# Optimization experiments

Measured on AMD Instinct MI355X. Metric: run time of the kernel, lower is better.

The kernel has to match this reference:

```python
import jax, jax.numpy as jnp
import numpy as np

B, N, C, H, S = 8, 1024, 768, 8, 16  # C = 3 * S * S, head_dim = C // H
NCH = 3
D = C // H
SCALE = D ** -0.5
REATTEN_SCALE = 1.0  # transform_scale=False
EPS = 1e-5  # BatchNorm2d eps


def conv3x3(x, w, b):
    # x: (B*N, 3, S, S); w: (O=3, I=3, 3, 3) OIHW; 'same' padding
    y = jax.lax.conv_general_dilated(x, w, (1, 1), 'SAME',
                                     dimension_numbers=('NCHW', 'OIHW', 'NCHW'))
    return y + b[None, :, None, None]


def setup_inputs() -> dict:
    key = jax.random.key(0)
    ks = jax.random.split(key, 8)
    return {
        'x': jax.random.normal(ks[0], (B, N, C), jnp.float32),
        'qw': jax.random.normal(ks[1], (NCH, NCH, 3, 3), jnp.float32) * 0.1,
        'qb': jnp.zeros((NCH,), jnp.float32),
        'kw': jax.random.normal(ks[2], (NCH, NCH, 3, 3), jnp.float32) * 0.1,
        'kb': jnp.zeros((NCH,), jnp.float32),
        'vw': jax.random.normal(ks[3], (NCH, NCH, 3, 3), jnp.float32) * 0.1,
        'vb': jnp.zeros((NCH,), jnp.float32),
        'rw': jax.random.normal(ks[4], (H, H), jnp.float32) * 0.2,  # 1x1 conv over heads
        'rb': jnp.zeros((H,), jnp.float32),
        'bn_g': jnp.ones((H,), jnp.float32),
        'bn_b': jnp.zeros((H,), jnp.float32),
        'bn_m': jnp.zeros((H,), jnp.float32),   # running mean
        'bn_v': jnp.ones((H,), jnp.float32),    # running var
        'pw': jax.random.normal(ks[5], (C, C), jnp.float32) * 0.02,
        'pb': jnp.zeros((C,), jnp.float32),
    }


def reference(x, qw, qb, kw, kb, vw, vb, rw, rb, bn_g, bn_b, bn_m, bn_v, pw, pb):
    Bx, Nx, Cx = x.shape
    xs = x.reshape(Bx * Nx, NCH, S, S)  # unflatten; all (b, n) convs batched at once

    def heads(y):  # (B*N, 3, S, S) -> (B, H, N, D)
        return y.reshape(Bx, Nx, H, D).transpose(0, 2, 1, 3)

    q = heads(conv3x3(xs, qw, qb))
    k = heads(conv3x3(xs, kw, kb))
    v = heads(conv3x3(xs, vw, vb))

    attn = jnp.einsum('bhnd,bhmd->bhnm', q, k) * SCALE  # (B, H, N, N)
    attn = jax.nn.softmax(attn, axis=-1)
    # re-attention: 1x1 conv across heads, then BatchNorm2d (eval, running stats)
    attn = jnp.einsum('oh,bhnm->bonm', rw, attn) + rb[None, :, None, None]
    inv = (bn_g / jnp.sqrt(bn_v + EPS))[None, :, None, None]
    attn = (attn - bn_m[None, :, None, None]) * inv + bn_b[None, :, None, None]
    attn = attn * REATTEN_SCALE

    out = jnp.einsum('bhnm,bhmd->bhnd', attn, v)  # (B, H, N, D)
    out = out.transpose(0, 2, 1, 3).reshape(Bx, Nx, Cx)
    out = out @ pw.T + pb
    return (out, attn)
```

## Files before the change

### kernel.cpp

```cpp
#include <hip/hip_runtime.h>
#include <math.h>

#define B_ 8
#define N_ 1024
#define C_ 768
#define H_ 8
#define D_ 96
#define SCALE_F 0.1020620726159657f

typedef unsigned short u16;
typedef __bf16 bf16x8 __attribute__((ext_vector_type(8)));
typedef float f32x4 __attribute__((ext_vector_type(4)));
typedef u16 u16x8 __attribute__((ext_vector_type(8)));

#define MFMA(a, b, c) __builtin_amdgcn_mfma_f32_16x16x32_bf16(a, b, c, 0, 0, 0)

__device__ inline void split1(float x, u16& h, u16& l) {
    __bf16 hb = (__bf16)x;
    float hf = (float)hb;
    __bf16 lb = (__bf16)(x - hf);
    h = __builtin_bit_cast(u16, hb);
    l = __builtin_bit_cast(u16, lb);
}

__device__ inline void split4(float4 x, ushort4& h, ushort4& l) {
    split1(x.x, h.x, l.x);
    split1(x.y, h.y, l.y);
    split1(x.z, h.z, l.z);
    split1(x.w, h.w, l.w);
}

__device__ inline void bar_lds() {
    asm volatile("s_waitcnt lgkmcnt(0)" ::: "memory");
    __builtin_amdgcn_s_barrier();
}

__device__ inline float bf16_to_f32(u16 u) {
    return __builtin_bit_cast(float, (unsigned)u << 16);
}

__global__ __launch_bounds__(256) void conv_qkv(
    const float* __restrict__ x,
    const float* __restrict__ qw, const float* __restrict__ qb,
    const float* __restrict__ kw, const float* __restrict__ kb,
    const float* __restrict__ vw, const float* __restrict__ vb,
    u16* __restrict__ qh, u16* __restrict__ ql,
    u16* __restrict__ kh, u16* __restrict__ kl,
    float* __restrict__ v)
{
    __shared__ float simg[768];
    __shared__ float sw[243];
    __shared__ float sb[9];
    const int img = blockIdx.x;
    const int b = img >> 10;
    const int tid = threadIdx.x;

    for (int i = tid; i < 768; i += 256) simg[i] = x[(size_t)img * 768 + i];
    if (tid < 243) {
        int g = tid / 81, i = tid % 81;
        const float* w = (g == 0) ? qw : (g == 1) ? kw : vw;
        sw[tid] = w[i];
    }
    if (tid < 9) {
        int g = tid / 3, i = tid % 3;
        const float* bb = (g == 0) ? qb : (g == 1) ? kb : vb;
        sb[tid] = bb[i];
    }
    __syncthreads();

    const int n = img & 1023;
    for (int e = tid; e < 2304; e += 256) {
        int g = e / 768, c = e % 768;
        int oc = c >> 8, rem = c & 255, y = rem >> 4, xx = rem & 15;
        float acc = sb[g * 3 + oc];
        const float* wg = &sw[g * 81 + oc * 27];
        #pragma unroll
        for (int ic = 0; ic < 3; ++ic)
            #pragma unroll
            for (int ky = 0; ky < 3; ++ky) {
                int yy = y + ky - 1;
                if (yy < 0 || yy > 15) continue;
                #pragma unroll
                for (int kx = 0; kx < 3; ++kx) {
                    int xp = xx + kx - 1;
                    if (xp < 0 || xp > 15) continue;
                    acc += wg[ic * 9 + ky * 3 + kx] * simg[ic * 256 + yy * 16 + xp];
                }
            }
        int hh = c / 96, d = c % 96;
        size_t o = ((size_t)(b * 8 + hh) * 1024 + n) * 96 + d;
        if (g == 2) {
            v[o] = acc;
        } else {
            u16 hi, lo;
            split1(acc, hi, lo);
            if (g == 0) { qh[o] = hi; ql[o] = lo; }
            else        { kh[o] = hi; kl[o] = lo; }
        }
    }
}

__global__ __launch_bounds__(256) void vt_split(
    const float* __restrict__ v, u16* __restrict__ vt_h)
{
    __shared__ float t32[32][36];
    const int bh = blockIdx.z, n0 = blockIdx.x * 32, d0 = blockIdx.y * 32;
    const int tid = threadIdx.x;
    {
        int nn = tid >> 3, c4 = (tid & 7) * 4;
        float4 x = *(const float4*)&v[((size_t)bh * 1024 + n0 + nn) * 96 + d0 + c4];
        t32[nn][c4] = x.x; t32[nn][c4 + 1] = x.y;
        t32[nn][c4 + 2] = x.z; t32[nn][c4 + 3] = x.w;
    }
    __syncthreads();
    {
        int d = tid >> 3, n4 = (tid & 7) * 4;
        ushort4 h;
        h.x = __builtin_bit_cast(u16, (__bf16)t32[n4][d]);
        h.y = __builtin_bit_cast(u16, (__bf16)t32[n4 + 1][d]);
        h.z = __builtin_bit_cast(u16, (__bf16)t32[n4 + 2][d]);
        h.w = __builtin_bit_cast(u16, (__bf16)t32[n4 + 3][d]);
        size_t o = ((size_t)bh * 96 + d0 + d) * 1024 + n0 + n4;
        *(ushort4*)&vt_h[o] = h;
    }
}

__global__ __launch_bounds__(256) void pw_split(
    const float* __restrict__ pw, u16* __restrict__ pwh, u16* __restrict__ pwl)
{
    int i = blockIdx.x * 256 + threadIdx.x;
    float4 x = *(const float4*)&pw[(size_t)i * 4];
    ushort4 h, l;
    split4(x, h, l);
    *(ushort4*)&pwh[(size_t)i * 4] = h;
    *(ushort4*)&pwl[(size_t)i * 4] = l;
}

__global__ __launch_bounds__(512) void fused_attn(
    const u16* __restrict__ qh, const u16* __restrict__ ql,
    const u16* __restrict__ kh, const u16* __restrict__ kl,
    const u16* __restrict__ vth,
    const float* __restrict__ rw, const float* __restrict__ rb,
    const float* __restrict__ bn_g, const float* __restrict__ bn_b,
    const float* __restrict__ bn_m, const float* __restrict__ bn_v,
    float* __restrict__ attn, u16* __restrict__ o1h, u16* __restrict__ o1l)
{
    __shared__ u16 p_lds[2][32][33][8];
    __shared__ u16 m_lds[2][8][32][40];
    __shared__ float s_w2[8][8];
    __shared__ float s_b2[8];

    const int bid = blockIdx.x;
    const int b = bid & 7;
    const int n0 = (bid >> 3) * 32;
    const int tid = threadIdx.x, wid = tid >> 6, lane = tid & 63;
    const int l16 = lane & 15, kg = lane >> 4;
    const int h = wid;
    const size_t bh = (size_t)(b * 8 + h);

    if (tid < 64) {
        int o = tid >> 3, hh = tid & 7;
        float inv = bn_g[o] * rsqrtf(bn_v[o] + 1e-5f);
        s_w2[o][hh] = rw[o * 8 + hh] * inv;
        if (hh == 0) s_b2[o] = (rb[o] - bn_m[o]) * inv + bn_b[o];
    }

    bf16x8 qhf[2][3], qlf[2][3];
    #pragma unroll
    for (int nf = 0; nf < 2; ++nf)
        #pragma unroll
        for (int ks = 0; ks < 3; ++ks) {
            size_t off = (bh * 1024 + n0 + nf * 16 + l16) * 96 + ks * 32 + kg * 8;
            qhf[nf][ks] = *(const bf16x8*)&qh[off];
            qlf[nf][ks] = *(const bf16x8*)&ql[off];
        }

    float ls[2][4];
    #pragma unroll
    for (int nf = 0; nf < 2; ++nf)
        #pragma unroll
        for (int r = 0; r < 4; ++r) ls[nf][r] = 0.f;

    #pragma unroll 1
    for (int mt = 0; mt < 16; ++mt) {
        const int m0 = mt * 64;
        f32x4 sacc[2][4];
        #pragma unroll
        for (int nf = 0; nf < 2; ++nf)
            #pragma unroll
            for (int mf = 0; mf < 4; ++mf) sacc[nf][mf] = (f32x4){0.f, 0.f, 0.f, 0.f};

        __builtin_amdgcn_s_setprio(1);
        #pragma unroll
        for (int ks = 0; ks < 3; ++ks) {
            bf16x8 kbh[4];
            #pragma unroll
            for (int mf = 0; mf < 4; ++mf) {
                size_t off = (bh * 1024 + m0 + mf * 16 + l16) * 96 + ks * 32 + kg * 8;
                kbh[mf] = *(const bf16x8*)&kh[off];
            }
            #pragma unroll
            for (int nf = 0; nf < 2; ++nf)
                #pragma unroll
                for (int mf = 0; mf < 4; ++mf)
                    sacc[nf][mf] = MFMA(qhf[nf][ks], kbh[mf], sacc[nf][mf]);
        }
        __builtin_amdgcn_s_setprio(0);

        #pragma unroll
        for (int nf = 0; nf < 2; ++nf)
            #pragma unroll
            for (int mf = 0; mf < 4; ++mf)
                #pragma unroll
                for (int r = 0; r < 4; ++r)
                    ls[nf][r] += __expf(sacc[nf][mf][r] * SCALE_F);
    }

    float rv[2][4];
    #pragma unroll
    for (int nf = 0; nf < 2; ++nf)
        #pragma unroll
        for (int r = 0; r < 4; ++r) {
            float s = ls[nf][r];
            #pragma unroll
            for (int off = 1; off < 16; off <<= 1) s += __shfl_xor(s, off);
            rv[nf][r] = 1.0f / s;
        }

    __syncthreads();

    float w2all[8][8], b2r[8];
    #pragma unroll
    for (int o = 0; o < 8; ++o) {
        b2r[o] = s_b2[o];
        #pragma unroll
        for (int hh = 0; hh < 8; ++hh) w2all[o][hh] = s_w2[o][hh];
    }

    f32x4 pvacc[2][6];
    #pragma unroll
    for (int nf = 0; nf < 2; ++nf)
        #pragma unroll
        for (int df = 0; df < 6; ++df) pvacc[nf][df] = (f32x4){0.f, 0.f, 0.f, 0.f};

    const int mm = lane & 31, halfq = lane >> 5;
    const int nlA = wid * 4 + halfq;
    const int nlB = wid * 4 + 2 + halfq;

#define QKEXP(MT, BUF)                                                          \
    {                                                                           \
        const int m0_ = (MT) * 32;                                              \
        f32x4 sacc_[2][2];                                                      \
        _Pragma("unroll")                                                       \
        for (int nf_ = 0; nf_ < 2; ++nf_)                                       \
            _Pragma("unroll")                                                   \
            for (int mf_ = 0; mf_ < 2; ++mf_)                                   \
                sacc_[nf_][mf_] = (f32x4){0.f, 0.f, 0.f, 0.f};                  \
        __builtin_amdgcn_s_setprio(1);                                          \
        _Pragma("unroll")                                                       \
        for (int ks_ = 0; ks_ < 3; ++ks_) {                                     \
            bf16x8 kbh_[2], kbl_[2];                                            \
            _Pragma("unroll")                                                   \
            for (int mf_ = 0; mf_ < 2; ++mf_) {                                 \
                size_t off_ = (bh * 1024 + m0_ + mf_ * 16 + l16) * 96 + ks_ * 32 + kg * 8; \
                kbh_[mf_] = *(const bf16x8*)&kh[off_];                          \
                kbl_[mf_] = *(const bf16x8*)&kl[off_];                          \
            }                                                                   \
            _Pragma("unroll")                                                   \
            for (int nf_ = 0; nf_ < 2; ++nf_)                                   \
                _Pragma("unroll")                                               \
                for (int mf_ = 0; mf_ < 2; ++mf_) {                             \
                    sacc_[nf_][mf_] = MFMA(qhf[nf_][ks_], kbh_[mf_], sacc_[nf_][mf_]); \
                    sacc_[nf_][mf_] = MFMA(qhf[nf_][ks_], kbl_[mf_], sacc_[nf_][mf_]); \
                    sacc_[nf_][mf_] = MFMA(qlf[nf_][ks_], kbh_[mf_], sacc_[nf_][mf_]); \
                }                                                               \
        }                                                                       \
        __builtin_amdgcn_s_setprio(0);                                          \
        _Pragma("unroll")                                                       \
        for (int nf_ = 0; nf_ < 2; ++nf_)                                       \
            _Pragma("unroll")                                                   \
            for (int mf_ = 0; mf_ < 2; ++mf_)                                   \
                _Pragma("unroll")                                               \
                for (int r_ = 0; r_ < 4; ++r_) {                                \
                    float pp_ = __expf(sacc_[nf_][mf_][r_] * SCALE_F) * rv[nf_][r_]; \
                    p_lds[BUF][nf_ * 16 + kg * 4 + r_][mf_ * 16 + l16][h] =     \
                        __builtin_bit_cast(u16, (__bf16)pp_);                   \
                }                                                               \
    }

    QKEXP(0, 0)
    bar_lds();

    #pragma unroll 1
    for (int mt = 0; mt < 32; ++mt) {
        const int m0 = mt * 32;
        const int buf = mt & 1;

        bf16x8 vbh[6];
        #pragma unroll
        for (int df = 0; df < 6; ++df) {
            size_t off = (bh * 96 + df * 16 + l16) * 1024 + m0 + kg * 8;
            vbh[df] = *(const bf16x8*)&vth[off];
        }

        if (mt < 31) QKEXP(mt + 1, buf ^ 1)

        {
            u16x8 pa = *(const u16x8*)&p_lds[buf][nlA][mm][0];
            u16x8 pb = *(const u16x8*)&p_lds[buf][nlB][mm][0];
            float macc[2][8];
            #pragma unroll
            for (int o = 0; o < 8; ++o) { macc[0][o] = b2r[o]; macc[1][o] = b2r[o]; }
            #pragma unroll
            for (int hh = 0; hh < 8; ++hh) {
                float pA = bf16_to_f32(pa[hh]);
                float pB = bf16_to_f32(pb[hh]);
                #pragma unroll
                for (int o = 0; o < 8; ++o) {
                    macc[0][o] += w2all[o][hh] * pA;
                    macc[1][o] += w2all[o][hh] * pB;
                }
            }
            #pragma unroll
            for (int o = 0; o < 8; ++o) {
                size_t basео = ((size_t)(b * 8 + o) * 1024 + n0);
                __builtin_nontemporal_store(macc[0][o],
                    &attn[(basео + nlA) * 1024 + m0 + mm]);
                __builtin_nontemporal_store(macc[1][o],
                    &attn[(basео + nlB) * 1024 + m0 + mm]);
                m_lds[buf][o][nlA][mm] = __builtin_bit_cast(u16, (__bf16)macc[0][o]);
                m_lds[buf][o][nlB][mm] = __builtin_bit_cast(u16, (__bf16)macc[1][o]);
            }
        }

        bar_lds();

        bf16x8 mah[2];
        #pragma unroll
        for (int nf = 0; nf < 2; ++nf)
            mah[nf] = __builtin_bit_cast(bf16x8,
                *(const u16x8*)&m_lds[buf][wid][nf * 16 + l16][kg * 8]);
        __builtin_amdgcn_s_setprio(1);
        #pragma unroll
        for (int df = 0; df < 6; ++df)
            #pragma unroll
            for (int nf = 0; nf < 2; ++nf)
                pvacc[nf][df] = MFMA(mah[nf], vbh[df], pvacc[nf][df]);
        __builtin_amdgcn_s_setprio(0);
    }
#undef QKEXP

    #pragma unroll
    for (int nf = 0; nf < 2; ++nf)
        #pragma unroll
        for (int df = 0; df < 6; ++df)
            #pragma unroll
            for (int r = 0; r < 4; ++r) {
                int row = n0 + nf * 16 + kg * 4 + r;
                int col = h * 96 + df * 16 + l16;
                u16 hh2, ll2;
                split1(pvacc[nf][df][r], hh2, ll2);
                size_t o = ((size_t)b * 1024 + row) * 768 + col;
                o1h[o] = hh2;
                o1l[o] = ll2;
            }
}

__global__ __launch_bounds__(256) void proj_mfma(
    const u16* __restrict__ o1h, const u16* __restrict__ o1l,
    const u16* __restrict__ pwh, const u16* __restrict__ pwl,
    const float* __restrict__ pb, float* __restrict__ out)
{
    __shared__ __align__(16) u16 Ahs[5120], Als[5120];
    __shared__ __align__(16) u16 Bhs[2560], Bls[2560];
    const int t0 = blockIdx.y * 128, o0 = blockIdx.x * 64;
    const int tid = threadIdx.x;
    const int wid = tid >> 6, lane = tid & 63;
    const int l16 = lane & 15, kg = lane >> 4;
    const int wr = wid >> 1, wc = wid & 1;

    f32x4 acc[4][2];
    #pragma unroll
    for (int i = 0; i < 4; ++i)
        #pragma unroll
        for (int j = 0; j < 2; ++j) acc[i][j] = (f32x4){0.f, 0.f, 0.f, 0.f};

    for (int s = 0; s < 24; ++s) {
        const int kc = s * 32;
        if (s) __syncthreads();
        #pragma unroll
        for (int i = 0; i < 4; ++i) {
            int idx = tid + i * 256;
            int r = idx >> 3, c4 = idx & 7;
            *(ushort4*)&Ahs[r * 40 + c4 * 4] = *(const ushort4*)&o1h[(size_t)(t0 + r) * 768 + kc + c4 * 4];
            *(ushort4*)&Als[r * 40 + c4 * 4] = *(const ushort4*)&o1l[(size_t)(t0 + r) * 768 + kc + c4 * 4];
        }
        #pragma unroll
        for (int i = 0; i < 2; ++i) {
            int idx = tid + i * 256;
            int r = idx >> 3, c4 = idx & 7;
            *(ushort4*)&Bhs[r * 40 + c4 * 4] = *(const ushort4*)&pwh[(size_t)(o0 + r) * 768 + kc + c4 * 4];
            *(ushort4*)&Bls[r * 40 + c4 * 4] = *(const ushort4*)&pwl[(size_t)(o0 + r) * 768 + kc + c4 * 4];
        }
        __syncthreads();

        bf16x8 ah[4], al[4], bh8[2], bl8[2];
        #pragma unroll
        for (int f = 0; f < 4; ++f) {
            int ra = (wr * 64 + f * 16 + l16) * 40 + kg * 8;
            ah[f] = *(const bf16x8*)&Ahs[ra];
            al[f] = *(const bf16x8*)&Als[ra];
        }
        #pragma unroll
        for (int j = 0; j < 2; ++j) {
            int rb = (wc * 32 + j * 16 + l16) * 40 + kg * 8;
            bh8[j] = *(const bf16x8*)&Bhs[rb];
            bl8[j] = *(const bf16x8*)&Bls[rb];
        }
        #pragma unroll
        for (int i = 0; i < 4; ++i)
            #pragma unroll
            for (int j = 0; j < 2; ++j) {
                acc[i][j] = MFMA(ah[i], bh8[j], acc[i][j]);
                acc[i][j] = MFMA(ah[i], bl8[j], acc[i][j]);
                acc[i][j] = MFMA(al[i], bh8[j], acc[i][j]);
            }
    }

    #pragma unroll
    for (int i = 0; i < 4; ++i) {
        int rr = t0 + wr * 64 + i * 16 + kg * 4;
        #pragma unroll
        for (int j = 0; j < 2; ++j) {
            int cc = o0 + wc * 32 + j * 16 + l16;
            float bias = pb[cc];
            #pragma unroll
            for (int r = 0; r < 4; ++r)
                __builtin_nontemporal_store(acc[i][j][r] + bias,
                                            &out[(size_t)(rr + r) * 768 + cc]);
        }
    }
}

extern "C" void kernel_launch(void* const* d_in, const int* in_sizes, int n_in,
                              void* d_out, int out_size, void* d_ws, size_t ws_size,
                              hipStream_t stream)
{
    const float* x    = (const float*)d_in[0];
    const float* qw   = (const float*)d_in[1];
    const float* qb   = (const float*)d_in[2];
    const float* kw   = (const float*)d_in[3];
    const float* kb   = (const float*)d_in[4];
    const float* vw   = (const float*)d_in[5];
    const float* vb   = (const float*)d_in[6];
    const float* rw   = (const float*)d_in[7];
    const float* rb   = (const float*)d_in[8];
    const float* bn_g = (const float*)d_in[9];
    const float* bn_b = (const float*)d_in[10];
    const float* bn_m = (const float*)d_in[11];
    const float* bn_v = (const float*)d_in[12];
    const float* pw   = (const float*)d_in[13];
    const float* pb   = (const float*)d_in[14];

    float* out_p  = (float*)d_out;
    float* attn_p = out_p + (size_t)B_ * N_ * C_;

    float* ws = (float*)d_ws;
    const size_t qkv = (size_t)B_ * H_ * N_ * D_;

    float* vf  = ws;
    u16* qhp = (u16*)(ws + qkv);
    u16* qlp = qhp + qkv;
    u16* khp = qlp + qkv;
    u16* klp = khp + qkv;
    u16* vth = (u16*)(ws + 3 * qkv);
    u16* o1h = (u16*)(ws + 4 * qkv);
    u16* o1l = o1h + qkv;
    u16* pwh = (u16*)(ws + 5 * qkv);
    u16* pwl = pwh + (size_t)C_ * C_;

    conv_qkv<<<B_ * N_, 256, 0, stream>>>(x, qw, qb, kw, kb, vw, vb,
                                          qhp, qlp, khp, klp, vf);
    vt_split<<<dim3(32, 3, 64), 256, 0, stream>>>(vf, vth);
    pw_split<<<576, 256, 0, stream>>>(pw, pwh, pwl);
    fused_attn<<<256, 512, 0, stream>>>(qhp, qlp, khp, klp, vth,
                                        rw, rb, bn_g, bn_b, bn_m, bn_v,
                                        attn_p, o1h, o1l);
    proj_mfma<<<dim3(12, 64), 256, 0, stream>>>(o1h, o1l, pwh, pwl, pb, out_p);
}
```

Before: 324.4 us.

## Defer PV MFMA by one tile and keep softmax probabilities in fp32 LDS

Moves the P·V MFMA step for tile mt-1 after the QK/exp of tile mt+1 and before the re-attention mix, so there is one fewer barrier-separated phase per iteration and MFMA work overlaps the scalar mixing. The softmax probabilities are now stored in LDS as fp32 in a head-major layout, replacing packed bf16, which removes the bf16 rounding before the head mix and changes the thread-to-row mapping. The cost is a larger LDS footprint and more LDS read traffic. The double-buffered m_lds must stay valid for one extra iteration.

```diff
diff --git a/kernel.cpp b/kernel.cpp
--- a/kernel.cpp
+++ b/kernel.cpp
@@ -33,10 +33,6 @@
 __device__ inline void bar_lds() {
     asm volatile("s_waitcnt lgkmcnt(0)" ::: "memory");
     __builtin_amdgcn_s_barrier();
-}
-
-__device__ inline float bf16_to_f32(u16 u) {
-    return __builtin_bit_cast(float, (unsigned)u << 16);
 }
 
 __global__ __launch_bounds__(256) void conv_qkv(
@@ -145,7 +141,7 @@
     const float* __restrict__ bn_m, const float* __restrict__ bn_v,
     float* __restrict__ attn, u16* __restrict__ o1h, u16* __restrict__ o1l)
 {
-    __shared__ u16 p_lds[2][32][33][8];
+    __shared__ float p_lds[2][8][32][36];
     __shared__ u16 m_lds[2][8][32][40];
     __shared__ float s_w2[8][8];
     __shared__ float s_b2[8];
@@ -243,9 +239,8 @@
         #pragma unroll
         for (int df = 0; df < 6; ++df) pvacc[nf][df] = (f32x4){0.f, 0.f, 0.f, 0.f};
 
-    const int mm = lane & 31, halfq = lane >> 5;
-    const int nlA = wid * 4 + halfq;
-    const int nlB = wid * 4 + 2 + halfq;
+    const int mm = tid & 31;
+    const int nl = (tid >> 5) & 15;
 
 #define QKEXP(MT, BUF)                                                          \
     {                                                                           \
@@ -283,9 +278,30 @@
                 _Pragma("unroll")                                               \
                 for (int r_ = 0; r_ < 4; ++r_) {                                \
                     float pp_ = __expf(sacc_[nf_][mf_][r_] * SCALE_F) * rv[nf_][r_]; \
-                    p_lds[BUF][nf_ * 16 + kg * 4 + r_][mf_ * 16 + l16][h] =     \
-                        __builtin_bit_cast(u16, (__bf16)pp_);                   \
+                    p_lds[BUF][h][nf_ * 16 + kg * 4 + r_][mf_ * 16 + l16] = pp_; \
                 }                                                               \
+    }
+
+#define PV_STEP(MB, M0V)                                                        \
+    {                                                                           \
+        bf16x8 vbh_[6];                                                         \
+        _Pragma("unroll")                                                       \
+        for (int df_ = 0; df_ < 6; ++df_) {                                     \
+            size_t off_ = (bh * 96 + df_ * 16 + l16) * 1024 + (M0V) + kg * 8;   \
+            vbh_[df_] = *(const bf16x8*)&vth[off_];                             \
+        }                                                                       \
+        bf16x8 mah_[2];                                                         \
+        _Pragma("unroll")                                                       \
+        for (int nf_ = 0; nf_ < 2; ++nf_)                                       \
+            mah_[nf_] = __builtin_bit_cast(bf16x8,                              \
+                *(const u16x8*)&m_lds[MB][h][nf_ * 16 + l16][kg * 8]);          \
+        __builtin_amdgcn_s_setprio(1);                                          \
+        _Pragma("unroll")                                                       \
+        for (int df_ = 0; df_ < 6; ++df_)                                       \
+            _Pragma("unroll")                                                   \
+            for (int nf_ = 0; nf_ < 2; ++nf_)                                   \
+                pvacc[nf_][df_] = MFMA(mah_[nf_], vbh_[df_], pvacc[nf_][df_]);  \
+        __builtin_amdgcn_s_setprio(0);                                          \
     }
 
     QKEXP(0, 0)
@@ -296,59 +312,38 @@
         const int m0 = mt * 32;
         const int buf = mt & 1;
 
-        bf16x8 vbh[6];
-        #pragma unroll
-        for (int df = 0; df < 6; ++df) {
-            size_t off = (bh * 96 + df * 16 + l16) * 1024 + m0 + kg * 8;
-            vbh[df] = *(const bf16x8*)&vth[off];
-        }
-
         if (mt < 31) QKEXP(mt + 1, buf ^ 1)
 
+        if (mt > 0) PV_STEP(buf ^ 1, m0 - 32)
+
         {
-            u16x8 pa = *(const u16x8*)&p_lds[buf][nlA][mm][0];
-            u16x8 pb = *(const u16x8*)&p_lds[buf][nlB][mm][0];
-            float macc[2][8];
-            #pragma unroll
-            for (int o = 0; o < 8; ++o) { macc[0][o] = b2r[o]; macc[1][o] = b2r[o]; }
+            float pA[8], pB[8];
             #pragma unroll
             for (int hh = 0; hh < 8; ++hh) {
-                float pA = bf16_to_f32(pa[hh]);
-                float pB = bf16_to_f32(pb[hh]);
+                pA[hh] = p_lds[buf][hh][nl][mm];
+                pB[hh] = p_lds[buf][hh][nl + 16][mm];
+            }
+            #pragma unroll
+            for (int o = 0; o < 8; ++o) {
+                float a = b2r[o], c = b2r[o];
                 #pragma unroll
-                for (int o = 0; o < 8; ++o) {
-                    macc[0][o] += w2all[o][hh] * pA;
-                    macc[1][o] += w2all[o][hh] * pB;
+                for (int hh = 0; hh < 8; ++hh) {
+                    a += w2all[o][hh] * pA[hh];
+                    c += w2all[o][hh] * pB[hh];
                 }
-            }
-            #pragma unroll
-            for (int o = 0; o < 8; ++o) {
-                size_t basео = ((size_t)(b * 8 + o) * 1024 + n0);
-                __builtin_nontemporal_store(macc[0][o],
-                    &attn[(basео + nlA) * 1024 + m0 + mm]);
-                __builtin_nontemporal_store(macc[1][o],
-                    &attn[(basео + nlB) * 1024 + m0 + mm]);
-                m_lds[buf][o][nlA][mm] = __builtin_bit_cast(u16, (__bf16)macc[0][o]);
-                m_lds[buf][o][nlB][mm] = __builtin_bit_cast(u16, (__bf16)macc[1][o]);
+                size_t baseo = ((size_t)(b * 8 + o) * 1024 + n0);
+                __builtin_nontemporal_store(a, &attn[(baseo + nl) * 1024 + m0 + mm]);
+                __builtin_nontemporal_store(c, &attn[(baseo + nl + 16) * 1024 + m0 + mm]);
+                m_lds[buf][o][nl][mm]      = __builtin_bit_cast(u16, (__bf16)a);
+                m_lds[buf][o][nl + 16][mm] = __builtin_bit_cast(u16, (__bf16)c);
             }
         }
 
         bar_lds();
-
-        bf16x8 mah[2];
-        #pragma unroll
-        for (int nf = 0; nf < 2; ++nf)
-            mah[nf] = __builtin_bit_cast(bf16x8,
-                *(const u16x8*)&m_lds[buf][wid][nf * 16 + l16][kg * 8]);
-        __builtin_amdgcn_s_setprio(1);
-        #pragma unroll
-        for (int df = 0; df < 6; ++df)
-            #pragma unroll
-            for (int nf = 0; nf < 2; ++nf)
-                pvacc[nf][df] = MFMA(mah[nf], vbh[df], pvacc[nf][df]);
-        __builtin_amdgcn_s_setprio(0);
-    }
+    }
+    PV_STEP(1, 31 * 32)
 #undef QKEXP
+#undef PV_STEP
 
     #pragma unroll
     for (int nf = 0; nf < 2; ++nf)
```

After: 309.3 us. 4.6% less time.
